# Kernel tuning notes

Measured on AMD Instinct MI355X. Metric: run time of the kernel, lower is better.

## Reference

```python
import jax, jax.numpy as jnp
import numpy as np

B, C_IN, C_OUT, H, W = 16, 64, 64, 192, 192
K_DY, KS, STRIDE, PAD = 4, 3, 1, 1
TEMP = 30.0
HID = int(C_IN * 0.25) + 1  # 17, matches hidden_channels rule for in_channels != 3
GROUPS = 8
EPS = 1e-5
NEG_SLOPE = 0.01


def setup_inputs() -> dict:
    key = jax.random.key(0)
    ks = jax.random.split(key, 6)
    return {
        "x": jax.random.normal(ks[0], (B, C_IN, H, W), jnp.float32),
        "attn_w1": jax.random.normal(ks[1], (HID, C_IN), jnp.float32) * 0.1,   # 1x1 conv, no bias
        "attn_w2": jax.random.normal(ks[2], (K_DY, HID), jnp.float32) * 0.1,   # 1x1 conv
        "attn_b2": jnp.zeros((K_DY,), jnp.float32),
        "weights": jax.random.normal(ks[3], (K_DY, C_OUT, C_IN, KS, KS), jnp.float32),
        "gn_gamma": jnp.ones((C_OUT,), jnp.float32),
        "gn_beta": jnp.zeros((C_OUT,), jnp.float32),
    }


def reference(x, attn_w1, attn_w2, attn_b2, weights, gn_gamma, gn_beta):
    b = x.shape[0]
    # SE-style attention over the dynamic-filter bank
    pooled = x.mean(axis=(2, 3))                       # (b, c_in) global avg pool
    h = jax.nn.relu(pooled @ attn_w1.T)                # (b, hid)
    scores = h @ attn_w2.T + attn_b2                   # (b, K)
    attn = jax.nn.softmax(scores / TEMP, axis=1)       # (b, K)
    # Per-sample synthesized filters
    filters = jnp.einsum('bk,koihw->boihw', attn, weights)   # (b, out_c, in_c, kh, kw)
    filters = filters.reshape(b * C_OUT, C_IN, KS, KS)
    # Grouped conv: groups = batch, each sample convolved with its own filter
    xg = x.reshape(1, b * C_IN, H, W)
    y = jax.lax.conv_general_dilated(
        xg, filters,
        window_strides=(STRIDE, STRIDE),
        padding=[(PAD, PAD), (PAD, PAD)],
        dimension_numbers=('NCHW', 'OIHW', 'NCHW'),
        feature_group_count=b,
    )
    y = y.reshape(b, C_OUT, y.shape[2], y.shape[3])
    # GroupNorm(8 groups) + LeakyReLU
    yg = y.reshape(b, GROUPS, C_OUT // GROUPS, y.shape[2], y.shape[3])
    mean = yg.mean(axis=(2, 3, 4), keepdims=True)
    var = yg.var(axis=(2, 3, 4), keepdims=True)
    yn = ((yg - mean) * jax.lax.rsqrt(var + EPS)).reshape(y.shape)
    yn = yn * gn_gamma[None, :, None, None] + gn_beta[None, :, None, None]
    return jnp.where(yn >= 0, yn, NEG_SLOPE * yn)
```

## Files before the change

kernel.cpp:

```cpp
#include <hip/hip_runtime.h>

typedef unsigned short u16;
typedef unsigned int u32;
typedef _Float16 f16;
typedef __attribute__((ext_vector_type(8))) f16 v8h;
typedef __attribute__((ext_vector_type(4))) f16 v4h;
typedef __attribute__((ext_vector_type(16))) float v16f;

#define BN 16
#define CHN 64
#define HH 192
#define WW 192
#define HWSZ 36864
#define KDY 4
#define HIDN 17
#define NG 8
#define TEMP_ 30.0f
#define EPSV 1e-5f
#define NSLOPE 0.01f
#define NTILE 144

#define TR 4
#define TC 32
#define HR 6
#define HC 34
#define PSTR 34
#define ROWH (HC * PSTR * 2)
#define NCHUNK (HR * HC * 8)
#define NBLK 4608
#define TAPH 4096

__device__ float g_pp[BN * NTILE * CHN];
__device__ float g_attn[BN * KDY];
__device__ float g_stats[BN * NG * 2];
__device__ __align__(16) f16 g_filt[BN * 9 * TAPH];
__device__ __align__(16) f16 g_xh[(size_t)BN * HWSZ * CHN];
__device__ __align__(16) f16 g_yh[(size_t)BN * CHN * HWSZ];

__global__ void __launch_bounds__(256) trans_pool_kernel(const float* __restrict__ x) {
    __shared__ u32 ts[256 * 34];
    const int b = blockIdx.y, tile = blockIdx.x;
    const int t = threadIdx.x;
    const int p0 = tile * 256;
    const float* xb = x + (size_t)b * CHN * HWSZ + p0;
    #pragma unroll 4
    for (int cp = 0; cp < 32; cp++) {
        float v0 = xb[(size_t)(2 * cp) * HWSZ + t];
        float v1 = xb[(size_t)(2 * cp + 1) * HWSZ + t];
        u32 pk = (u32)__builtin_bit_cast(u16, (f16)v0)
               | ((u32)__builtin_bit_cast(u16, (f16)v1) << 16);
        ts[t * 34 + cp] = pk;
    }
    __syncthreads();
    f16* dp = g_xh + ((size_t)b * HWSZ + p0 + t) * CHN;
    const u32* src = ts + t * 34;
    #pragma unroll
    for (int i = 0; i < 8; i++) {
        uint2 a = *(const uint2*)(src + 4 * i);
        uint2 c = *(const uint2*)(src + 4 * i + 2);
        ((uint4*)dp)[i] = make_uint4(a.x, a.y, c.x, c.y);
    }
    const int cp = t & 31, seg = t >> 5;
    float s0 = 0.f, s1 = 0.f;
    for (int p = 0; p < 32; p++) {
        u32 pk = ts[(seg * 32 + p) * 34 + cp];
        s0 += (float)__builtin_bit_cast(f16, (u16)(pk & 0xffffu));
        s1 += (float)__builtin_bit_cast(f16, (u16)(pk >> 16));
    }
    s0 += __shfl_down(s0, 32);
    s1 += __shfl_down(s1, 32);
    __syncthreads();
    float* ps = (float*)ts;
    const int lane = t & 63, w = t >> 6;
    if (lane < 32) { ps[(w * 32 + lane) * 2] = s0; ps[(w * 32 + lane) * 2 + 1] = s1; }
    __syncthreads();
    if (t < 32) {
        float a0 = ps[t * 2] + ps[(32 + t) * 2] + ps[(64 + t) * 2] + ps[(96 + t) * 2];
        float a1 = ps[t * 2 + 1] + ps[(32 + t) * 2 + 1]
                 + ps[(64 + t) * 2 + 1] + ps[(96 + t) * 2 + 1];
        float* gp = g_pp + ((size_t)b * NTILE + tile) * CHN;
        gp[2 * t] = a0; gp[2 * t + 1] = a1;
    }
}

__global__ void __launch_bounds__(256) attn_kernel(const float* __restrict__ w1,
                                                   const float* __restrict__ w2,
                                                   const float* __restrict__ b2) {
    __shared__ float red[256];
    __shared__ float pr[CHN];
    __shared__ float hs[HIDN];
    const int b = blockIdx.x, t = threadIdx.x;
    if (t < NG * 2) g_stats[b * NG * 2 + t] = 0.f;
    const int c = t & 63, part = t >> 6;
    const float* gp = g_pp + (size_t)b * NTILE * CHN + c;
    float s = 0.f;
    #pragma unroll 4
    for (int i = part * 36; i < part * 36 + 36; i++) s += gp[i * CHN];
    red[t] = s;
    __syncthreads();
    if (t < CHN)
        pr[t] = (red[t] + red[t + 64] + red[t + 128] + red[t + 192]) * (1.0f / HWSZ);
    __syncthreads();
    if (t < HIDN) {
        float a = 0.f;
        for (int cc = 0; cc < CHN; cc++) a += w1[t * CHN + cc] * pr[cc];
        hs[t] = fmaxf(a, 0.f);
    }
    __syncthreads();
    if (t == 0) {
        float scv[KDY]; float m = -3e38f;
        #pragma unroll
        for (int k = 0; k < KDY; k++) {
            float sc = b2[k];
            for (int h = 0; h < HIDN; h++) sc += w2[k * HIDN + h] * hs[h];
            sc *= (1.0f / TEMP_);
            scv[k] = sc; m = fmaxf(m, sc);
        }
        float den = 0.f;
        #pragma unroll
        for (int k = 0; k < KDY; k++) { scv[k] = __expf(scv[k] - m); den += scv[k]; }
        float rd = 1.f / den;
        #pragma unroll
        for (int k = 0; k < KDY; k++) g_attn[b * KDY + k] = scv[k] * rd;
    }
}

__global__ void filt_kernel(const float* __restrict__ wts) {
    __shared__ float at[BN * KDY];
    if (threadIdx.x < BN * KDY) at[threadIdx.x] = g_attn[threadIdx.x];
    __syncthreads();
    int t = blockIdx.x * 256 + threadIdx.x;
    int tap = t / 4096;
    int co = (t >> 6) & 63;
    int ci = t & 63;
    float w0 = wts[((0 * CHN + co) * CHN + ci) * 9 + tap];
    float w1 = wts[((1 * CHN + co) * CHN + ci) * 9 + tap];
    float w2 = wts[((2 * CHN + co) * CHN + ci) * 9 + tap];
    float w3 = wts[((3 * CHN + co) * CHN + ci) * 9 + tap];
    const int wc = co >> 5, n = co & 31;
    const int kb = ci >> 4, rest = ci & 15;
    const size_t dst = (size_t)tap * TAPH + wc * 2048 + kb * 512 + n * 16 + rest;
    #pragma unroll
    for (int b = 0; b < BN; b++) {
        float v = at[b * 4] * w0 + at[b * 4 + 1] * w1
                + at[b * 4 + 2] * w2 + at[b * 4 + 3] * w3;
        g_filt[(size_t)b * 9 * TAPH + dst] = (f16)v;
    }
}

__global__ void __launch_bounds__(256, 5) conv_kernel() {
    __shared__ __align__(16) u32 xs[HR * HC * PSTR];
    __shared__ float gsum[NG], gsq[NG];
    const int bid = blockIdx.x;
    const int swz = (bid & 7) * 576 + (bid >> 3);
    const int b = swz / 288;
    const int rem = swz - b * 288;
    const int r0 = (rem / 6) * TR, c0 = (rem % 6) * TC;
    const int tid = threadIdx.x;
    const int w = tid >> 6, lane = tid & 63;
    const int wr = w >> 1, wc = w & 1;
    const int n = lane & 31, hi = lane >> 5;
    if (tid < NG) { gsum[tid] = 0.f; gsq[tid] = 0.f; }

    const f16* xhb = g_xh + (size_t)b * HWSZ * CHN;
    uint4 rv[7];
    #pragma unroll
    for (int i = 0; i < 7; i++) {
        int l = tid + i * 256;
        int pix = l >> 3, part = l & 7;
        int hr = pix / HC, hc = pix - hr * HC;
        int gr = r0 - 1 + hr, gc = c0 - 1 + hc;
        bool ok = (l < NCHUNK) && ((unsigned)gr < HH) && ((unsigned)gc < WW);
        size_t off = ok ? ((size_t)(gr * WW + gc) * CHN + part * 8) : 0;
        rv[i] = *(const uint4*)(xhb + off);
    }
    #pragma unroll
    for (int i = 0; i < 7; i++) {
        int l = tid + i * 256;
        if (l < NCHUNK) {
            int pix = l >> 3, part = l & 7;
            int hr = pix / HC, hc = pix - hr * HC;
            int gr = r0 - 1 + hr, gc = c0 - 1 + hc;
            bool ok = ((unsigned)gr < HH) && ((unsigned)gc < WW);
            uint4 v = ok ? rv[i] : make_uint4(0, 0, 0, 0);
            u32* d = xs + pix * PSTR + part * 4;
            *(uint2*)d = make_uint2(v.x, v.y);
            *(uint2*)(d + 2) = make_uint2(v.z, v.w);
        }
    }
    __syncthreads();

    const f16* xsh = (const f16*)xs;
    const f16* fb = g_filt + (size_t)b * 9 * TAPH + wc * 2048 + n * 16 + hi * 8;
    v16f acc0 = {}, acc1 = {};

    v8h A[9][4];
    #pragma unroll
    for (int kb = 0; kb < 4; kb++) {
        A[0][kb] = *(const v8h*)(fb + kb * 512);
        A[1][kb] = *(const v8h*)(fb + TAPH + kb * 512);
    }
    #pragma unroll
    for (int tap = 0; tap < 9; tap++) {
        if (tap < 7) {
            const f16* fp = fb + (size_t)(tap + 2) * TAPH;
            #pragma unroll
            for (int kb = 0; kb < 4; kb++) A[tap + 2][kb] = *(const v8h*)(fp + kb * 512);
        }
        const int dy = tap / 3, dx = tap - 3 * (tap / 3);
        const f16* xr = xsh + ((2 * wr + dy) * HC + (n + dx)) * (PSTR * 2) + hi * 8;
        __builtin_amdgcn_s_setprio(1);
        #pragma unroll
        for (int kb = 0; kb < 4; kb++) {
            v4h lo0 = *(const v4h*)(xr + kb * 16);
            v4h up0 = *(const v4h*)(xr + kb * 16 + 4);
            v4h lo1 = *(const v4h*)(xr + kb * 16 + ROWH);
            v4h up1 = *(const v4h*)(xr + kb * 16 + 4 + ROWH);
            v8h b0 = __builtin_shufflevector(lo0, up0, 0, 1, 2, 3, 4, 5, 6, 7);
            v8h b1 = __builtin_shufflevector(lo1, up1, 0, 1, 2, 3, 4, 5, 6, 7);
            acc0 = __builtin_amdgcn_mfma_f32_32x32x16_f16(A[tap][kb], b0, acc0, 0, 0, 0);
            acc1 = __builtin_amdgcn_mfma_f32_32x32x16_f16(A[tap][kb], b1, acc1, 0, 0, 0);
        }
        __builtin_amdgcn_s_setprio(0);
    }

    float sg[4] = {0.f, 0.f, 0.f, 0.f}, sq[4] = {0.f, 0.f, 0.f, 0.f};
    f16* yb = g_yh + (size_t)b * CHN * HWSZ + (size_t)(r0 + 2 * wr) * WW + (c0 + n);
    #pragma unroll
    for (int r = 0; r < 16; r++) {
        int co = wc * 32 + (r & 3) + 8 * (r >> 2) + 4 * hi;
        float a0 = acc0[r], a1 = acc1[r];
        yb[(size_t)co * HWSZ] = (f16)a0;
        yb[(size_t)co * HWSZ + WW] = (f16)a1;
        int gl = r >> 2;
        sg[gl] += a0 + a1; sq[gl] += a0 * a0 + a1 * a1;
    }
    #pragma unroll
    for (int gl = 0; gl < 4; gl++) {
        float s = sg[gl], q = sq[gl];
        #pragma unroll
        for (int off = 32; off > 0; off >>= 1) {
            s += __shfl_down(s, off);
            q += __shfl_down(q, off);
        }
        if (lane == 0) { atomicAdd(&gsum[4 * wc + gl], s); atomicAdd(&gsq[4 * wc + gl], q); }
    }
    __syncthreads();
    if (tid < 2 * NG) {
        int g = tid >> 1, which = tid & 1;
        atomicAdd(&g_stats[(b * NG + g) * 2 + which], which ? gsq[g] : gsum[g]);
    }
}

__global__ void __launch_bounds__(256) norm_kernel(float* __restrict__ out,
                                                   const float* __restrict__ gamma,
                                                   const float* __restrict__ beta) {
    const int tid = threadIdx.x;
    const float invN = 1.0f / (8.0f * HWSZ);
    #pragma unroll
    for (int it = 0; it < 8; it++) {
        int ch = it * 2304 + blockIdx.x;
        int bco = ch / 18;
        int b = bco >> 6, co = bco & 63;
        int g = co >> 3;
        float mean = g_stats[(b * NG + g) * 2 + 0] * invN;
        float var = fmaxf(g_stats[(b * NG + g) * 2 + 1] * invN - mean * mean, 0.f);
        float sc = rsqrtf(var + EPSV) * gamma[co];
        float sh = beta[co] - mean * sc;
        size_t base = (size_t)ch * 2048 + tid * 8;
        v8h v = *(const v8h*)(g_yh + base);
        float vv[8];
        #pragma unroll
        for (int t = 0; t < 8; t++) {
            float a = (float)v[t] * sc + sh;
            vv[t] = a >= 0.f ? a : NSLOPE * a;
        }
        float4* op = (float4*)(out + base);
        op[0] = make_float4(vv[0], vv[1], vv[2], vv[3]);
        op[1] = make_float4(vv[4], vv[5], vv[6], vv[7]);
    }
}

extern "C" void kernel_launch(void* const* d_in, const int* in_sizes, int n_in,
                              void* d_out, int out_size, void* d_ws, size_t ws_size,
                              hipStream_t stream) {
    const float* x     = (const float*)d_in[0];
    const float* w1    = (const float*)d_in[1];
    const float* w2    = (const float*)d_in[2];
    const float* b2    = (const float*)d_in[3];
    const float* wts   = (const float*)d_in[4];
    const float* gamma = (const float*)d_in[5];
    const float* beta  = (const float*)d_in[6];
    float* out = (float*)d_out;

    dim3 tg(NTILE, BN);
    trans_pool_kernel<<<tg, 256, 0, stream>>>(x);
    attn_kernel<<<BN, 256, 0, stream>>>(w1, w2, b2);
    filt_kernel<<<144, 256, 0, stream>>>(wts);
    conv_kernel<<<NBLK, 256, 0, stream>>>();
    norm_kernel<<<2304, 256, 0, stream>>>(out, gamma, beta);
}
```

Baseline: 377.6 us.

## Fuse attention into filter kernel and batch loads in transpose and norm kernels

Merges the attention kernel into the filter-synthesis kernel, so each of the 144 blocks recomputes pooling, MLP and softmax for all batches redundantly instead of paying for a separate launch. The GroupNorm stats zeroing moves into the transpose kernel. The transpose-pool and norm kernels now issue all their global loads up front to raise memory-level parallelism, at the cost of more registers per thread.

```diff
diff --git a/kernel.cpp b/kernel.cpp
--- a/kernel.cpp
+++ b/kernel.cpp
@@ -31,7 +31,6 @@
 #define TAPH 4096
 
 __device__ float g_pp[BN * NTILE * CHN];
-__device__ float g_attn[BN * KDY];
 __device__ float g_stats[BN * NG * 2];
 __device__ __align__(16) f16 g_filt[BN * 9 * TAPH];
 __device__ __align__(16) f16 g_xh[(size_t)BN * HWSZ * CHN];
@@ -41,14 +40,19 @@
     __shared__ u32 ts[256 * 34];
     const int b = blockIdx.y, tile = blockIdx.x;
     const int t = threadIdx.x;
+    if (tile == 0 && t < NG * 2) g_stats[b * NG * 2 + t] = 0.f;
     const int p0 = tile * 256;
     const float* xb = x + (size_t)b * CHN * HWSZ + p0;
-    #pragma unroll 4
+    float v0[32], v1[32];
+    #pragma unroll
     for (int cp = 0; cp < 32; cp++) {
-        float v0 = xb[(size_t)(2 * cp) * HWSZ + t];
-        float v1 = xb[(size_t)(2 * cp + 1) * HWSZ + t];
-        u32 pk = (u32)__builtin_bit_cast(u16, (f16)v0)
-               | ((u32)__builtin_bit_cast(u16, (f16)v1) << 16);
+        v0[cp] = xb[(size_t)(2 * cp) * HWSZ + t];
+        v1[cp] = xb[(size_t)(2 * cp + 1) * HWSZ + t];
+    }
+    #pragma unroll
+    for (int cp = 0; cp < 32; cp++) {
+        u32 pk = (u32)__builtin_bit_cast(u16, (f16)v0[cp])
+               | ((u32)__builtin_bit_cast(u16, (f16)v1[cp]) << 16);
         ts[t * 34 + cp] = pk;
     }
     __syncthreads();
@@ -83,36 +87,45 @@
     }
 }
 
-__global__ void __launch_bounds__(256) attn_kernel(const float* __restrict__ w1,
+__global__ void __launch_bounds__(256) filt_kernel(const float* __restrict__ w1,
                                                    const float* __restrict__ w2,
-                                                   const float* __restrict__ b2) {
-    __shared__ float red[256];
-    __shared__ float pr[CHN];
-    __shared__ float hs[HIDN];
-    const int b = blockIdx.x, t = threadIdx.x;
-    if (t < NG * 2) g_stats[b * NG * 2 + t] = 0.f;
-    const int c = t & 63, part = t >> 6;
-    const float* gp = g_pp + (size_t)b * NTILE * CHN + c;
-    float s = 0.f;
-    #pragma unroll 4
-    for (int i = part * 36; i < part * 36 + 36; i++) s += gp[i * CHN];
-    red[t] = s;
-    __syncthreads();
-    if (t < CHN)
-        pr[t] = (red[t] + red[t + 64] + red[t + 128] + red[t + 192]) * (1.0f / HWSZ);
-    __syncthreads();
-    if (t < HIDN) {
+                                                   const float* __restrict__ b2,
+                                                   const float* __restrict__ wts) {
+    __shared__ float pooled[BN][CHN];
+    __shared__ float hsm[BN][HIDN];
+    __shared__ float at[BN * KDY];
+    const int tt = threadIdx.x;
+    {
+        int bb = tt >> 4, cb = (tt & 15) * 4;
+        const float* gp = g_pp + (size_t)bb * NTILE * CHN + cb;
+        float4 a = make_float4(0.f, 0.f, 0.f, 0.f);
+        for (int i = 0; i < NTILE; i++) {
+            float4 v = *(const float4*)(gp + (size_t)i * CHN);
+            a.x += v.x; a.y += v.y; a.z += v.z; a.w += v.w;
+        }
+        const float s = 1.0f / HWSZ;
+        pooled[bb][cb] = a.x * s; pooled[bb][cb + 1] = a.y * s;
+        pooled[bb][cb + 2] = a.z * s; pooled[bb][cb + 3] = a.w * s;
+    }
+    __syncthreads();
+    {
+        int bb = tt >> 4, h = tt & 15;
         float a = 0.f;
-        for (int cc = 0; cc < CHN; cc++) a += w1[t * CHN + cc] * pr[cc];
-        hs[t] = fmaxf(a, 0.f);
-    }
-    __syncthreads();
-    if (t == 0) {
+        for (int c = 0; c < CHN; c++) a += w1[h * CHN + c] * pooled[bb][c];
+        hsm[bb][h] = fmaxf(a, 0.f);
+        if (tt < BN) {
+            float a2 = 0.f;
+            for (int c = 0; c < CHN; c++) a2 += w1[16 * CHN + c] * pooled[tt][c];
+            hsm[tt][16] = fmaxf(a2, 0.f);
+        }
+    }
+    __syncthreads();
+    if (tt < BN) {
         float scv[KDY]; float m = -3e38f;
         #pragma unroll
         for (int k = 0; k < KDY; k++) {
             float sc = b2[k];
-            for (int h = 0; h < HIDN; h++) sc += w2[k * HIDN + h] * hs[h];
+            for (int h = 0; h < HIDN; h++) sc += w2[k * HIDN + h] * hsm[tt][h];
             sc *= (1.0f / TEMP_);
             scv[k] = sc; m = fmaxf(m, sc);
         }
@@ -121,29 +134,24 @@
         for (int k = 0; k < KDY; k++) { scv[k] = __expf(scv[k] - m); den += scv[k]; }
         float rd = 1.f / den;
         #pragma unroll
-        for (int k = 0; k < KDY; k++) g_attn[b * KDY + k] = scv[k] * rd;
-    }
-}
-
-__global__ void filt_kernel(const float* __restrict__ wts) {
-    __shared__ float at[BN * KDY];
-    if (threadIdx.x < BN * KDY) at[threadIdx.x] = g_attn[threadIdx.x];
-    __syncthreads();
-    int t = blockIdx.x * 256 + threadIdx.x;
+        for (int k = 0; k < KDY; k++) at[tt * KDY + k] = scv[k] * rd;
+    }
+    __syncthreads();
+    int t = blockIdx.x * 256 + tt;
     int tap = t / 4096;
     int co = (t >> 6) & 63;
     int ci = t & 63;
     float w0 = wts[((0 * CHN + co) * CHN + ci) * 9 + tap];
-    float w1 = wts[((1 * CHN + co) * CHN + ci) * 9 + tap];
-    float w2 = wts[((2 * CHN + co) * CHN + ci) * 9 + tap];
-    float w3 = wts[((3 * CHN + co) * CHN + ci) * 9 + tap];
+    float wv1 = wts[((1 * CHN + co) * CHN + ci) * 9 + tap];
+    float wv2 = wts[((2 * CHN + co) * CHN + ci) * 9 + tap];
+    float wv3 = wts[((3 * CHN + co) * CHN + ci) * 9 + tap];
     const int wc = co >> 5, n = co & 31;
     const int kb = ci >> 4, rest = ci & 15;
     const size_t dst = (size_t)tap * TAPH + wc * 2048 + kb * 512 + n * 16 + rest;
     #pragma unroll
     for (int b = 0; b < BN; b++) {
-        float v = at[b * 4] * w0 + at[b * 4 + 1] * w1
-                + at[b * 4 + 2] * w2 + at[b * 4 + 3] * w3;
+        float v = at[b * 4] * w0 + at[b * 4 + 1] * wv1
+                + at[b * 4 + 2] * wv2 + at[b * 4 + 3] * wv3;
         g_filt[(size_t)b * 9 * TAPH + dst] = (f16)v;
     }
 }
@@ -257,6 +265,7 @@
                                                    const float* __restrict__ beta) {
     const int tid = threadIdx.x;
     const float invN = 1.0f / (8.0f * HWSZ);
+    v8h v[8]; float scv[8], shv[8];
     #pragma unroll
     for (int it = 0; it < 8; it++) {
         int ch = it * 2304 + blockIdx.x;
@@ -266,13 +275,18 @@
         float mean = g_stats[(b * NG + g) * 2 + 0] * invN;
         float var = fmaxf(g_stats[(b * NG + g) * 2 + 1] * invN - mean * mean, 0.f);
         float sc = rsqrtf(var + EPSV) * gamma[co];
-        float sh = beta[co] - mean * sc;
+        scv[it] = sc;
+        shv[it] = beta[co] - mean * sc;
+        v[it] = *(const v8h*)(g_yh + (size_t)ch * 2048 + tid * 8);
+    }
+    #pragma unroll
+    for (int it = 0; it < 8; it++) {
+        int ch = it * 2304 + blockIdx.x;
         size_t base = (size_t)ch * 2048 + tid * 8;
-        v8h v = *(const v8h*)(g_yh + base);
         float vv[8];
         #pragma unroll
         for (int t = 0; t < 8; t++) {
-            float a = (float)v[t] * sc + sh;
+            float a = (float)v[it][t] * scv[it] + shv[it];
             vv[t] = a >= 0.f ? a : NSLOPE * a;
         }
         float4* op = (float4*)(out + base);
@@ -295,8 +309,7 @@
 
     dim3 tg(NTILE, BN);
     trans_pool_kernel<<<tg, 256, 0, stream>>>(x);
-    attn_kernel<<<BN, 256, 0, stream>>>(w1, w2, b2);
-    filt_kernel<<<144, 256, 0, stream>>>(wts);
+    filt_kernel<<<144, 256, 0, stream>>>(w1, w2, b2, wts);
     conv_kernel<<<NBLK, 256, 0, stream>>>();
     norm_kernel<<<2304, 256, 0, stream>>>(out, gamma, beta);
 }
```

Result: slower. 385.5 us (+2.1%).
